# Performance work log

Measured on AMD Instinct MI355X. Metric: run time of the kernel, lower is better.

Reference implementation:

```python
import jax, jax.numpy as jnp
import numpy as np

B = 256       # batch
H = 512       # latent_size == hidden_size == t_channels == o_channels
O_LEN = 512   # decode steps (output_shape[0])


def setup_inputs() -> dict:
    key = jax.random.key(0)
    ks = jax.random.split(key, 7)
    s = 1.0 / np.sqrt(H)
    u = lambda k, shp: jax.random.uniform(k, shp, jnp.float32, -s, s)
    return {
        "z": jax.random.normal(ks[0], (B, H), jnp.float32),
        "W_ih": u(ks[1], (4 * H, H)),   # PyTorch LSTM weight_ih_l0, gate order i,f,g,o
        "W_hh": u(ks[2], (4 * H, H)),
        "b_ih": u(ks[3], (4 * H,)),
        "b_hh": u(ks[4], (4 * H,)),
        "W_last": u(ks[5], (H, H)),     # nn.Linear(hidden_size, o_channels)
        "b_last": u(ks[6], (H,)),
    }


def reference(z, W_ih, W_hh, b_ih, b_hh, W_last, b_last):
    b = b_ih + b_hh

    def step(carry, _):
        x, h, c = carry  # each (B, H)
        gates = x @ W_ih.T + h @ W_hh.T + b  # (B, 4H)
        i, f, g, o = jnp.split(gates, 4, axis=-1)
        c = jax.nn.sigmoid(f) * c + jax.nn.sigmoid(i) * jnp.tanh(g)
        h = jax.nn.sigmoid(o) * jnp.tanh(c)
        y = h @ W_last.T + b_last  # (B, H) -> fed back as next input
        return (y, h, c), y

    # state = (z, z) as (h0, c0); first input x0 = z
    _, ys = jax.lax.scan(step, (z, z, z), None, length=O_LEN)  # ys: (O_LEN, B, H)
    return jnp.transpose(ys, (1, 0, 2))  # (B, O_LEN, H)
```

## Files before the change

kernel.cpp:

```cpp
#include <hip/hip_runtime.h>


#define HH 512
#define TT 512

typedef _Float16 half8 __attribute__((ext_vector_type(8)));
typedef float f32x4 __attribute__((ext_vector_type(4)));

__device__ __forceinline__ float sigm(float x) { return 1.0f / (1.0f + __expf(-x)); }
__device__ __forceinline__ float tanh_(float x) { return 1.0f - 2.0f / (__expf(2.0f * x) + 1.0f); }
__device__ __forceinline__ unsigned short f16b(float x) {
    _Float16 h = (_Float16)x;
    return __builtin_bit_cast(unsigned short, h);
}

__global__ __launch_bounds__(256) void k_weff(const float* __restrict__ Wih,
                                              const float* __restrict__ Whh,
                                              const float* __restrict__ Wlast,
                                              unsigned short* __restrict__ Wbig) {
    __shared__ float wih[16 * 512];
    const int tid = threadIdx.x;
    const int r0 = blockIdx.x * 16;
    for (int i = tid; i < (16 * 512) / 4; i += 256) {
        ((float4*)wih)[i] = ((const float4*)(Wih + (size_t)r0 * 512))[i];
    }
    __syncthreads();
    float acc0[16], acc1[16];
#pragma unroll
    for (int rr = 0; rr < 16; ++rr) { acc0[rr] = 0.f; acc1[rr] = 0.f; }
    const int k0 = tid * 2;
    for (int j = 0; j < 512; ++j) {
        const float2 wl = *(const float2*)(Wlast + (size_t)j * 512 + k0);
#pragma unroll
        for (int rr = 0; rr < 16; ++rr) {
            const float a = wih[rr * 512 + j];
            acc0[rr] += a * wl.x;
            acc1[rr] += a * wl.y;
        }
    }
#pragma unroll
    for (int rr = 0; rr < 16; ++rr) {
        const int gr = r0 + rr;
        const int q = gr >> 9, j = gr & 511;
        const int dst = 80 * (j >> 4) + q * 16 + (j & 15);
        const float v0 = acc0[rr] + Whh[(size_t)gr * 512 + k0];
        const float v1 = acc1[rr] + Whh[(size_t)gr * 512 + k0 + 1];
        Wbig[(size_t)dst * 512 + k0] = f16b(v0);
        Wbig[(size_t)dst * 512 + k0 + 1] = f16b(v1);
    }
}

__global__ __launch_bounds__(256) void k_pack(const float* __restrict__ z,
                                              const float* __restrict__ Wih,
                                              const float* __restrict__ Whh,
                                              const float* __restrict__ bih,
                                              const float* __restrict__ bhh,
                                              const float* __restrict__ Wlast,
                                              const float* __restrict__ blast,
                                              unsigned short* __restrict__ Wbig,
                                              unsigned short* __restrict__ W0big,
                                              float* __restrict__ biasEff,
                                              float* __restrict__ bias0,
                                              unsigned short* __restrict__ hbuf,
                                              unsigned int* __restrict__ counters) {
    const int nthr = gridDim.x * blockDim.x;
    const int gtid = blockIdx.x * blockDim.x + threadIdx.x;
    for (int e = gtid; e < 2560 * 512; e += nthr) {
        const int r = e >> 9, k = e & 511;
        const int s = r / 80, rem = r - s * 80;
        const int tau = rem >> 4, jj = rem & 15;
        const int j = s * 16 + jj;
        if (tau == 4) {
            const unsigned short v = f16b(Wlast[(size_t)j * 512 + k]);
            Wbig[e] = v;
            W0big[e] = v;
        } else {
            const int gr = tau * 512 + j;
            W0big[e] = f16b(Wih[(size_t)gr * 512 + k] + Whh[(size_t)gr * 512 + k]);
        }
    }
    for (int r = gtid; r < 2560; r += nthr) {
        const int s = r / 80, rem = r - s * 80;
        const int tau = rem >> 4, jj = rem & 15;
        const int j = s * 16 + jj;
        if (tau == 4) {
            bias0[r] = blast[j];
            biasEff[r] = blast[j];
        } else {
            const int gr = tau * 512 + j;
            const float base = bih[gr] + bhh[gr];
            float dot = 0.f;
            for (int k = 0; k < 512; ++k) dot += Wih[(size_t)gr * 512 + k] * blast[k];
            bias0[r] = base;
            biasEff[r] = base + dot;
        }
    }
    for (int e = gtid; e < 256 * 512; e += nthr) {
        const int b = e >> 9, k = e & 511;
        const int g = b >> 5, bl = b & 31;
        hbuf[((size_t)(g * 2) * 32 + bl) * 512 + k] = f16b(z[e]);
    }
    for (int e = gtid; e < 512; e += nthr) counters[e] = 0u;
}

__global__ __launch_bounds__(256, 1) void k_lstm(const unsigned short* __restrict__ Wbig,
                                                 const unsigned short* __restrict__ W0big,
                                                 const float* __restrict__ biasEff,
                                                 const float* __restrict__ bias0,
                                                 unsigned short* __restrict__ hbuf,
                                                 unsigned int* __restrict__ counters,
                                                 const float* __restrict__ z,
                                                 float* __restrict__ out) {
    const int g = blockIdx.x & 7;
    const int s = blockIdx.x >> 3;
    const int tid = threadIdx.x;
    const int wave = tid >> 6;
    const int lane = tid & 63;
    const int l15 = lane & 15;
    const int q4 = lane >> 4;

    __shared__ unsigned short hstage[32 * 520];
    __shared__ float gatesL[32 * 68];
    __shared__ float cL[32 * 18];

    const int mbase = (wave >> 1) * 16;
    const int ntile0 = (wave & 1) ? 3 : 0;
    const int ntcount = (wave & 1) ? 2 : 3;

    unsigned short* hb0 = hbuf + (size_t)(g * 2) * 32 * 512;
    unsigned short* hb1 = hb0 + 32 * 512;
    unsigned int* cnt = counters + g * 64;

    for (int idx = tid; idx < 512; idx += 256) {
        const int b = idx >> 4, jj = idx & 15;
        cL[b * 18 + jj] = z[(size_t)(g * 32 + b) * 512 + 16 * s + jj];
    }

    half8 bfrag[3][16];
#pragma unroll
    for (int tt = 0; tt < 3; ++tt) {
        if (tt < ntcount) {
            const int row = 80 * s + (ntile0 + tt) * 16 + l15;
#pragma unroll
            for (int kk = 0; kk < 16; ++kk) {
                bfrag[tt][kk] = *(const half8*)(W0big + (size_t)row * 512 + kk * 32 + q4 * 8);
            }
        }
    }
    float bias0v[3], biasEv[3];
#pragma unroll
    for (int tt = 0; tt < 3; ++tt) {
        if (tt < ntcount) {
            const int r = 80 * s + (ntile0 + tt) * 16 + l15;
            bias0v[tt] = bias0[r];
            biasEv[tt] = biasEff[r];
        } else {
            bias0v[tt] = 0.f;
            biasEv[tt] = 0.f;
        }
    }

    for (int t = 0; t <= 512; ++t) {
        {
            const unsigned short* src = (t & 1) ? hb1 : hb0;
            const char* p = (const char*)src + tid * 16;
            half8 st[8];
            asm volatile(
                "global_load_dwordx4 %0, %8, off sc0 sc1\n\t"
                "global_load_dwordx4 %1, %9, off sc0 sc1\n\t"
                "global_load_dwordx4 %2, %10, off sc0 sc1\n\t"
                "global_load_dwordx4 %3, %11, off sc0 sc1\n\t"
                "global_load_dwordx4 %4, %12, off sc0 sc1\n\t"
                "global_load_dwordx4 %5, %13, off sc0 sc1\n\t"
                "global_load_dwordx4 %6, %14, off sc0 sc1\n\t"
                "global_load_dwordx4 %7, %15, off sc0 sc1\n\t"
                "s_waitcnt vmcnt(0)"
                : "=&v"(st[0]), "=&v"(st[1]), "=&v"(st[2]), "=&v"(st[3]),
                  "=&v"(st[4]), "=&v"(st[5]), "=&v"(st[6]), "=&v"(st[7])
                : "v"(p), "v"(p + 4096), "v"(p + 8192), "v"(p + 12288),
                  "v"(p + 16384), "v"(p + 20480), "v"(p + 24576), "v"(p + 28672)
                : "memory");
#pragma unroll
            for (int i = 0; i < 8; ++i) {
                const int ci = i * 256 + tid;
                const int row = ci >> 6, col = ci & 63;
                *(half8*)(hstage + row * 520 + col * 8) = st[i];
            }
        }
        __syncthreads();

        f32x4 acc[3];
#pragma unroll
        for (int tt = 0; tt < 3; ++tt) {
            const float bv = (t == 0) ? bias0v[tt] : biasEv[tt];
            acc[tt] = (f32x4){bv, bv, bv, bv};
        }
#pragma unroll
        for (int kk = 0; kk < 16; ++kk) {
            const half8 a = *(const half8*)(hstage + (mbase + l15) * 520 + kk * 32 + q4 * 8);
#pragma unroll
            for (int tt = 0; tt < 3; ++tt) {
                if (tt < ntcount)
                    acc[tt] = __builtin_amdgcn_mfma_f32_16x16x32_f16(a, bfrag[tt][kk], acc[tt], 0, 0, 0);
            }
        }

        if ((wave & 1) && t >= 1) {
            const int n = 16 * s + l15;
#pragma unroll
            for (int r = 0; r < 4; ++r) {
                const int m = mbase + q4 * 4 + r;
                const size_t off = (size_t)(g * 32 + m) * (TT * HH) + (size_t)(t - 1) * HH + n;
                out[off] = acc[1][r];
            }
        }
        if (t == 512) break;

        {
            const int nst = (wave & 1) ? 1 : 3;
#pragma unroll
            for (int tt = 0; tt < 3; ++tt) {
                if (tt < nst) {
                    const int col = (ntile0 + tt) * 16 + l15;
#pragma unroll
                    for (int r = 0; r < 4; ++r) {
                        const int m = mbase + q4 * 4 + r;
                        gatesL[m * 68 + col] = acc[tt][r];
                    }
                }
            }
        }
        __syncthreads();

        {
            const int b = tid >> 3, jp = tid & 7;
            const int j0 = jp * 2;
            const float2 iv = *(const float2*)(gatesL + b * 68 + j0);
            const float2 fv = *(const float2*)(gatesL + b * 68 + 16 + j0);
            const float2 gv = *(const float2*)(gatesL + b * 68 + 32 + j0);
            const float2 ov = *(const float2*)(gatesL + b * 68 + 48 + j0);
            float2 cv = *(const float2*)(cL + b * 18 + j0);
            const float c0 = sigm(fv.x) * cv.x + sigm(iv.x) * tanh_(gv.x);
            const float c1 = sigm(fv.y) * cv.y + sigm(iv.y) * tanh_(gv.y);
            const float h0 = sigm(ov.x) * tanh_(c0);
            const float h1 = sigm(ov.y) * tanh_(c1);
            cv.x = c0;
            cv.y = c1;
            *(float2*)(cL + b * 18 + j0) = cv;
            unsigned short* dst = (t & 1) ? hb0 : hb1;
            const unsigned int packed = (unsigned int)f16b(h0) | ((unsigned int)f16b(h1) << 16);
            __hip_atomic_store((unsigned int*)(dst + b * 512 + 16 * s + j0), packed,
                               __ATOMIC_RELAXED, __HIP_MEMORY_SCOPE_AGENT);
        }

        if (t == 0) {
#pragma unroll
            for (int tt = 0; tt < 3; ++tt) {
                if (tt < ntcount) {
                    const int row = 80 * s + (ntile0 + tt) * 16 + l15;
#pragma unroll
                    for (int kk = 0; kk < 16; ++kk) {
                        bfrag[tt][kk] = *(const half8*)(Wbig + (size_t)row * 512 + kk * 32 + q4 * 8);
                    }
                }
            }
        }

        __syncthreads();
        if (tid == 0) {
            __hip_atomic_fetch_add(cnt, 1u, __ATOMIC_RELAXED, __HIP_MEMORY_SCOPE_AGENT);
            const unsigned int target = 32u * (unsigned)(t + 1);
            while (__hip_atomic_load(cnt, __ATOMIC_RELAXED, __HIP_MEMORY_SCOPE_AGENT) < target) {
            }
        }
        __syncthreads();
    }
}

extern "C" void kernel_launch(void* const* d_in, const int* in_sizes, int n_in,
                              void* d_out, int out_size, void* d_ws, size_t ws_size,
                              hipStream_t stream) {
    const float* z = (const float*)d_in[0];
    const float* Wih = (const float*)d_in[1];
    const float* Whh = (const float*)d_in[2];
    const float* bih = (const float*)d_in[3];
    const float* bhh = (const float*)d_in[4];
    const float* Wlast = (const float*)d_in[5];
    const float* blast = (const float*)d_in[6];
    float* out = (float*)d_out;

    char* ws = (char*)d_ws;
    unsigned short* Wbig = (unsigned short*)(ws);
    unsigned short* W0big = (unsigned short*)(ws + 2621440);
    float* biasEff = (float*)(ws + 5242880);
    float* bias0 = (float*)(ws + 5253120);
    unsigned short* hbuf = (unsigned short*)(ws + 5263360);
    unsigned int* counters = (unsigned int*)(ws + 5787648);

    k_weff<<<128, 256, 0, stream>>>(Wih, Whh, Wlast, Wbig);
    k_pack<<<512, 256, 0, stream>>>(z, Wih, Whh, bih, bhh, Wlast, blast, Wbig, W0big, biasEff,
                                    bias0, hbuf, counters);
    k_lstm<<<256, 256, 0, stream>>>(Wbig, W0big, biasEff, bias0, hbuf, counters, z, out);
}
```

Measured before the change: 2.251 ms.

## Keep LSTM gate tiles in registers per wave and halve the persistent block count

Each wave now computes all five 16-column tiles (i, f, g, o and the output projection) for its own hidden slice. The cell update therefore runs directly on MFMA accumulators, with the cell state held in registers instead of going through a shared-memory gates buffer. This removes one __syncthreads and the shared-memory round trip from every recurrent step. The grid shrinks from 256 to 128 blocks, so each group barrier waits for 16 arrivals instead of 32. Output stores move after the inter-block barrier so they can overlap the wait, and the spin loop gets an iteration cap, which risks a stale hidden-state read if the wait ever runs past the cap.

```diff
diff --git a/kernel.cpp b/kernel.cpp
--- a/kernel.cpp
+++ b/kernel.cpp
@@ -112,7 +112,7 @@
                                                  const float* __restrict__ z,
                                                  float* __restrict__ out) {
     const int g = blockIdx.x & 7;
-    const int s = blockIdx.x >> 3;
+    const int pair = blockIdx.x >> 3;
     const int tid = threadIdx.x;
     const int wave = tid >> 6;
     const int lane = tid & 63;
@@ -120,44 +120,36 @@
     const int q4 = lane >> 4;
 
     __shared__ unsigned short hstage[32 * 520];
-    __shared__ float gatesL[32 * 68];
-    __shared__ float cL[32 * 18];
-
-    const int mbase = (wave >> 1) * 16;
-    const int ntile0 = (wave & 1) ? 3 : 0;
-    const int ntcount = (wave & 1) ? 2 : 3;
+
+    const int slice = 2 * pair + (wave >> 1);
+    const int Mbase = (wave & 1) * 16;
+    const int jcol = 16 * slice + l15;
 
     unsigned short* hb0 = hbuf + (size_t)(g * 2) * 32 * 512;
     unsigned short* hb1 = hb0 + 32 * 512;
     unsigned int* cnt = counters + g * 64;
 
-    for (int idx = tid; idx < 512; idx += 256) {
-        const int b = idx >> 4, jj = idx & 15;
-        cL[b * 18 + jj] = z[(size_t)(g * 32 + b) * 512 + 16 * s + jj];
-    }
-
-    half8 bfrag[3][16];
-#pragma unroll
-    for (int tt = 0; tt < 3; ++tt) {
-        if (tt < ntcount) {
-            const int row = 80 * s + (ntile0 + tt) * 16 + l15;
-#pragma unroll
-            for (int kk = 0; kk < 16; ++kk) {
-                bfrag[tt][kk] = *(const half8*)(W0big + (size_t)row * 512 + kk * 32 + q4 * 8);
-            }
-        }
-    }
-    float bias0v[3], biasEv[3];
-#pragma unroll
-    for (int tt = 0; tt < 3; ++tt) {
-        if (tt < ntcount) {
-            const int r = 80 * s + (ntile0 + tt) * 16 + l15;
-            bias0v[tt] = bias0[r];
-            biasEv[tt] = biasEff[r];
-        } else {
-            bias0v[tt] = 0.f;
-            biasEv[tt] = 0.f;
-        }
+    float c_reg[4];
+#pragma unroll
+    for (int r = 0; r < 4; ++r) {
+        c_reg[r] = z[(size_t)(g * 32 + Mbase + q4 * 4 + r) * 512 + jcol];
+    }
+
+    half8 bfrag[5][16];
+#pragma unroll
+    for (int tt = 0; tt < 5; ++tt) {
+        const int row = 80 * slice + tt * 16 + l15;
+#pragma unroll
+        for (int kk = 0; kk < 16; ++kk) {
+            bfrag[tt][kk] = *(const half8*)(W0big + (size_t)row * 512 + kk * 32 + q4 * 8);
+        }
+    }
+    float bias0v[5], biasEv[5];
+#pragma unroll
+    for (int tt = 0; tt < 5; ++tt) {
+        const int r = 80 * slice + tt * 16 + l15;
+        bias0v[tt] = bias0[r];
+        biasEv[tt] = biasEff[r];
     }
 
     for (int t = 0; t <= 512; ++t) {
@@ -189,79 +181,53 @@
         }
         __syncthreads();
 
-        f32x4 acc[3];
-#pragma unroll
-        for (int tt = 0; tt < 3; ++tt) {
+        f32x4 acc[5];
+#pragma unroll
+        for (int tt = 0; tt < 5; ++tt) {
             const float bv = (t == 0) ? bias0v[tt] : biasEv[tt];
             acc[tt] = (f32x4){bv, bv, bv, bv};
         }
 #pragma unroll
         for (int kk = 0; kk < 16; ++kk) {
-            const half8 a = *(const half8*)(hstage + (mbase + l15) * 520 + kk * 32 + q4 * 8);
-#pragma unroll
-            for (int tt = 0; tt < 3; ++tt) {
-                if (tt < ntcount)
-                    acc[tt] = __builtin_amdgcn_mfma_f32_16x16x32_f16(a, bfrag[tt][kk], acc[tt], 0, 0, 0);
-            }
-        }
-
-        if ((wave & 1) && t >= 1) {
-            const int n = 16 * s + l15;
+            const half8 a = *(const half8*)(hstage + (Mbase + l15) * 520 + kk * 32 + q4 * 8);
+#pragma unroll
+            for (int tt = 0; tt < 5; ++tt) {
+                acc[tt] = __builtin_amdgcn_mfma_f32_16x16x32_f16(a, bfrag[tt][kk], acc[tt], 0, 0, 0);
+            }
+        }
+
+        if (t == 512) {
 #pragma unroll
             for (int r = 0; r < 4; ++r) {
-                const int m = mbase + q4 * 4 + r;
-                const size_t off = (size_t)(g * 32 + m) * (TT * HH) + (size_t)(t - 1) * HH + n;
-                out[off] = acc[1][r];
-            }
-        }
-        if (t == 512) break;
+                const size_t off = (size_t)(g * 32 + Mbase + q4 * 4 + r) * (TT * HH) +
+                                   (size_t)(t - 1) * HH + jcol;
+                out[off] = acc[4][r];
+            }
+            break;
+        }
 
         {
-            const int nst = (wave & 1) ? 1 : 3;
-#pragma unroll
-            for (int tt = 0; tt < 3; ++tt) {
-                if (tt < nst) {
-                    const int col = (ntile0 + tt) * 16 + l15;
-#pragma unroll
-                    for (int r = 0; r < 4; ++r) {
-                        const int m = mbase + q4 * 4 + r;
-                        gatesL[m * 68 + col] = acc[tt][r];
-                    }
-                }
-            }
-        }
-        __syncthreads();
-
-        {
-            const int b = tid >> 3, jp = tid & 7;
-            const int j0 = jp * 2;
-            const float2 iv = *(const float2*)(gatesL + b * 68 + j0);
-            const float2 fv = *(const float2*)(gatesL + b * 68 + 16 + j0);
-            const float2 gv = *(const float2*)(gatesL + b * 68 + 32 + j0);
-            const float2 ov = *(const float2*)(gatesL + b * 68 + 48 + j0);
-            float2 cv = *(const float2*)(cL + b * 18 + j0);
-            const float c0 = sigm(fv.x) * cv.x + sigm(iv.x) * tanh_(gv.x);
-            const float c1 = sigm(fv.y) * cv.y + sigm(iv.y) * tanh_(gv.y);
-            const float h0 = sigm(ov.x) * tanh_(c0);
-            const float h1 = sigm(ov.y) * tanh_(c1);
-            cv.x = c0;
-            cv.y = c1;
-            *(float2*)(cL + b * 18 + j0) = cv;
             unsigned short* dst = (t & 1) ? hb0 : hb1;
-            const unsigned int packed = (unsigned int)f16b(h0) | ((unsigned int)f16b(h1) << 16);
-            __hip_atomic_store((unsigned int*)(dst + b * 512 + 16 * s + j0), packed,
-                               __ATOMIC_RELAXED, __HIP_MEMORY_SCOPE_AGENT);
+#pragma unroll
+            for (int r = 0; r < 4; ++r) {
+                const float iv = acc[0][r], fv = acc[1][r], gv = acc[2][r], ov = acc[3][r];
+                const float c0 = sigm(fv) * c_reg[r] + sigm(iv) * tanh_(gv);
+                c_reg[r] = c0;
+                const float h0 = sigm(ov) * tanh_(c0);
+                unsigned short* pp = dst + (size_t)(Mbase + q4 * 4 + r) * 512 + jcol;
+                const unsigned short hv = f16b(h0);
+                asm volatile("global_store_short %0, %1, off sc0 sc1" ::"v"(pp), "v"(hv)
+                             : "memory");
+            }
         }
 
         if (t == 0) {
 #pragma unroll
-            for (int tt = 0; tt < 3; ++tt) {
-                if (tt < ntcount) {
-                    const int row = 80 * s + (ntile0 + tt) * 16 + l15;
-#pragma unroll
-                    for (int kk = 0; kk < 16; ++kk) {
-                        bfrag[tt][kk] = *(const half8*)(Wbig + (size_t)row * 512 + kk * 32 + q4 * 8);
-                    }
+            for (int tt = 0; tt < 4; ++tt) {
+                const int row = 80 * slice + tt * 16 + l15;
+#pragma unroll
+                for (int kk = 0; kk < 16; ++kk) {
+                    bfrag[tt][kk] = *(const half8*)(Wbig + (size_t)row * 512 + kk * 32 + q4 * 8);
                 }
             }
         }
@@ -269,11 +235,22 @@
         __syncthreads();
         if (tid == 0) {
             __hip_atomic_fetch_add(cnt, 1u, __ATOMIC_RELAXED, __HIP_MEMORY_SCOPE_AGENT);
-            const unsigned int target = 32u * (unsigned)(t + 1);
-            while (__hip_atomic_load(cnt, __ATOMIC_RELAXED, __HIP_MEMORY_SCOPE_AGENT) < target) {
+            const unsigned int target = 16u * (unsigned)(t + 1);
+            int guard = 0;
+            while (__hip_atomic_load(cnt, __ATOMIC_RELAXED, __HIP_MEMORY_SCOPE_AGENT) < target &&
+                   ++guard < 65536) {
             }
         }
         __syncthreads();
+
+        if (t >= 1) {
+#pragma unroll
+            for (int r = 0; r < 4; ++r) {
+                const size_t off = (size_t)(g * 32 + Mbase + q4 * 4 + r) * (TT * HH) +
+                                   (size_t)(t - 1) * HH + jcol;
+                out[off] = acc[4][r];
+            }
+        }
     }
 }
 
@@ -300,5 +277,5 @@
     k_weff<<<128, 256, 0, stream>>>(Wih, Whh, Wlast, Wbig);
     k_pack<<<512, 256, 0, stream>>>(z, Wih, Whh, bih, bhh, Wlast, blast, Wbig, W0big, biasEff,
                                     bias0, hbuf, counters);
-    k_lstm<<<256, 256, 0, stream>>>(Wbig, W0big, biasEff, bias0, hbuf, counters, z, out);
-}
+    k_lstm<<<128, 256, 0, stream>>>(Wbig, W0big, biasEff, bias0, hbuf, counters, z, out);
+}
```

Result: slower. 4.918 ms (+118.5%).

## Repartition LSTM blocks into 16 batch groups with two gate slices each

Applied to the files above, without the earlier changes.

Each persistent block now owns 16 batch rows and two 16-column hidden slices, instead of 32 batch rows and one slice. This halves the hidden-state rows each block must reload from global memory every step. It also halves the number of blocks in each group-wide spin barrier, from 32 to 16, to cut per-step synchronisation latency. The spin wait gains an iteration cap, which risks silently proceeding on stale state if a barrier is slow.

```diff
diff --git a/kernel.cpp b/kernel.cpp
--- a/kernel.cpp
+++ b/kernel.cpp
@@ -97,8 +97,8 @@
     }
     for (int e = gtid; e < 256 * 512; e += nthr) {
         const int b = e >> 9, k = e & 511;
-        const int g = b >> 5, bl = b & 31;
-        hbuf[((size_t)(g * 2) * 32 + bl) * 512 + k] = f16b(z[e]);
+        const int g = b >> 4, bl = b & 15;
+        hbuf[(size_t)g * 16384 + bl * 512 + k] = f16b(z[e]);
     }
     for (int e = gtid; e < 512; e += nthr) counters[e] = 0u;
 }
@@ -111,36 +111,38 @@
                                                  unsigned int* __restrict__ counters,
                                                  const float* __restrict__ z,
                                                  float* __restrict__ out) {
-    const int g = blockIdx.x & 7;
-    const int s = blockIdx.x >> 3;
+    const int g = blockIdx.x & 15;
+    const int pair = blockIdx.x >> 4;
     const int tid = threadIdx.x;
     const int wave = tid >> 6;
     const int lane = tid & 63;
     const int l15 = lane & 15;
     const int q4 = lane >> 4;
 
-    __shared__ unsigned short hstage[32 * 520];
-    __shared__ float gatesL[32 * 68];
-    __shared__ float cL[32 * 18];
-
-    const int mbase = (wave >> 1) * 16;
+    __shared__ unsigned short hstage[16 * 520];
+    __shared__ float gatesL[2 * 16 * 68];
+    __shared__ float cL[2 * 16 * 18];
+
+    const int sl = wave >> 1;
+    const int slice = 2 * pair + sl;
     const int ntile0 = (wave & 1) ? 3 : 0;
     const int ntcount = (wave & 1) ? 2 : 3;
 
-    unsigned short* hb0 = hbuf + (size_t)(g * 2) * 32 * 512;
-    unsigned short* hb1 = hb0 + 32 * 512;
-    unsigned int* cnt = counters + g * 64;
+    unsigned short* hb0 = hbuf + (size_t)g * 16384;
+    unsigned short* hb1 = hb0 + 8192;
+    unsigned int* cnt = counters + g * 32;
 
     for (int idx = tid; idx < 512; idx += 256) {
-        const int b = idx >> 4, jj = idx & 15;
-        cL[b * 18 + jj] = z[(size_t)(g * 32 + b) * 512 + 16 * s + jj];
+        const int b = idx >> 5, j0 = idx & 31;
+        const int s2 = j0 >> 4, jj = j0 & 15;
+        cL[(s2 * 16 + b) * 18 + jj] = z[(size_t)(g * 16 + b) * 512 + 32 * pair + j0];
     }
 
     half8 bfrag[3][16];
 #pragma unroll
     for (int tt = 0; tt < 3; ++tt) {
         if (tt < ntcount) {
-            const int row = 80 * s + (ntile0 + tt) * 16 + l15;
+            const int row = 80 * slice + (ntile0 + tt) * 16 + l15;
 #pragma unroll
             for (int kk = 0; kk < 16; ++kk) {
                 bfrag[tt][kk] = *(const half8*)(W0big + (size_t)row * 512 + kk * 32 + q4 * 8);
@@ -151,7 +153,7 @@
 #pragma unroll
     for (int tt = 0; tt < 3; ++tt) {
         if (tt < ntcount) {
-            const int r = 80 * s + (ntile0 + tt) * 16 + l15;
+            const int r = 80 * slice + (ntile0 + tt) * 16 + l15;
             bias0v[tt] = bias0[r];
             biasEv[tt] = biasEff[r];
         } else {
@@ -164,24 +166,18 @@
         {
             const unsigned short* src = (t & 1) ? hb1 : hb0;
             const char* p = (const char*)src + tid * 16;
-            half8 st[8];
+            half8 st[4];
             asm volatile(
-                "global_load_dwordx4 %0, %8, off sc0 sc1\n\t"
-                "global_load_dwordx4 %1, %9, off sc0 sc1\n\t"
-                "global_load_dwordx4 %2, %10, off sc0 sc1\n\t"
-                "global_load_dwordx4 %3, %11, off sc0 sc1\n\t"
-                "global_load_dwordx4 %4, %12, off sc0 sc1\n\t"
-                "global_load_dwordx4 %5, %13, off sc0 sc1\n\t"
-                "global_load_dwordx4 %6, %14, off sc0 sc1\n\t"
-                "global_load_dwordx4 %7, %15, off sc0 sc1\n\t"
+                "global_load_dwordx4 %0, %4, off sc0 sc1\n\t"
+                "global_load_dwordx4 %1, %5, off sc0 sc1\n\t"
+                "global_load_dwordx4 %2, %6, off sc0 sc1\n\t"
+                "global_load_dwordx4 %3, %7, off sc0 sc1\n\t"
                 "s_waitcnt vmcnt(0)"
-                : "=&v"(st[0]), "=&v"(st[1]), "=&v"(st[2]), "=&v"(st[3]),
-                  "=&v"(st[4]), "=&v"(st[5]), "=&v"(st[6]), "=&v"(st[7])
-                : "v"(p), "v"(p + 4096), "v"(p + 8192), "v"(p + 12288),
-                  "v"(p + 16384), "v"(p + 20480), "v"(p + 24576), "v"(p + 28672)
+                : "=&v"(st[0]), "=&v"(st[1]), "=&v"(st[2]), "=&v"(st[3])
+                : "v"(p), "v"(p + 4096), "v"(p + 8192), "v"(p + 12288)
                 : "memory");
 #pragma unroll
-            for (int i = 0; i < 8; ++i) {
+            for (int i = 0; i < 4; ++i) {
                 const int ci = i * 256 + tid;
                 const int row = ci >> 6, col = ci & 63;
                 *(half8*)(hstage + row * 520 + col * 8) = st[i];
@@ -197,7 +193,7 @@
         }
 #pragma unroll
         for (int kk = 0; kk < 16; ++kk) {
-            const half8 a = *(const half8*)(hstage + (mbase + l15) * 520 + kk * 32 + q4 * 8);
+            const half8 a = *(const half8*)(hstage + l15 * 520 + kk * 32 + q4 * 8);
 #pragma unroll
             for (int tt = 0; tt < 3; ++tt) {
                 if (tt < ntcount)
@@ -206,11 +202,12 @@
         }
 
         if ((wave & 1) && t >= 1) {
-            const int n = 16 * s + l15;
+            const int n = 16 * slice + l15;
 #pragma unroll
             for (int r = 0; r < 4; ++r) {
-                const int m = mbase + q4 * 4 + r;
-                const size_t off = (size_t)(g * 32 + m) * (TT * HH) + (size_t)(t - 1) * HH + n;
+                const int m = q4 * 4 + r;
+                const size_t off =
+                    (size_t)(g * 16 + m) * (TT * HH) + (size_t)(t - 1) * HH + n;
                 out[off] = acc[1][r];
             }
         }
@@ -224,8 +221,8 @@
                     const int col = (ntile0 + tt) * 16 + l15;
 #pragma unroll
                     for (int r = 0; r < 4; ++r) {
-                        const int m = mbase + q4 * 4 + r;
-                        gatesL[m * 68 + col] = acc[tt][r];
+                        const int m = q4 * 4 + r;
+                        gatesL[(sl * 16 + m) * 68 + col] = acc[tt][r];
                     }
                 }
             }
@@ -233,23 +230,26 @@
         __syncthreads();
 
         {
-            const int b = tid >> 3, jp = tid & 7;
+            const int b = tid >> 4, jp = tid & 15;
             const int j0 = jp * 2;
-            const float2 iv = *(const float2*)(gatesL + b * 68 + j0);
-            const float2 fv = *(const float2*)(gatesL + b * 68 + 16 + j0);
-            const float2 gv = *(const float2*)(gatesL + b * 68 + 32 + j0);
-            const float2 ov = *(const float2*)(gatesL + b * 68 + 48 + j0);
-            float2 cv = *(const float2*)(cL + b * 18 + j0);
-            const float c0 = sigm(fv.x) * cv.x + sigm(iv.x) * tanh_(gv.x);
-            const float c1 = sigm(fv.y) * cv.y + sigm(iv.y) * tanh_(gv.y);
+            const int s2 = j0 >> 4, jj = j0 & 15;
+            const float* gb = gatesL + (s2 * 16 + b) * 68;
+            const float2 iv = *(const float2*)(gb + jj);
+            const float2 fvv = *(const float2*)(gb + 16 + jj);
+            const float2 gv = *(const float2*)(gb + 32 + jj);
+            const float2 ov = *(const float2*)(gb + 48 + jj);
+            float* cp = cL + (s2 * 16 + b) * 18 + jj;
+            float2 cv = *(const float2*)cp;
+            const float c0 = sigm(fvv.x) * cv.x + sigm(iv.x) * tanh_(gv.x);
+            const float c1 = sigm(fvv.y) * cv.y + sigm(iv.y) * tanh_(gv.y);
             const float h0 = sigm(ov.x) * tanh_(c0);
             const float h1 = sigm(ov.y) * tanh_(c1);
             cv.x = c0;
             cv.y = c1;
-            *(float2*)(cL + b * 18 + j0) = cv;
+            *(float2*)cp = cv;
             unsigned short* dst = (t & 1) ? hb0 : hb1;
             const unsigned int packed = (unsigned int)f16b(h0) | ((unsigned int)f16b(h1) << 16);
-            __hip_atomic_store((unsigned int*)(dst + b * 512 + 16 * s + j0), packed,
+            __hip_atomic_store((unsigned int*)(dst + b * 512 + 32 * pair + j0), packed,
                                __ATOMIC_RELAXED, __HIP_MEMORY_SCOPE_AGENT);
         }
 
@@ -257,7 +257,7 @@
 #pragma unroll
             for (int tt = 0; tt < 3; ++tt) {
                 if (tt < ntcount) {
-                    const int row = 80 * s + (ntile0 + tt) * 16 + l15;
+                    const int row = 80 * slice + (ntile0 + tt) * 16 + l15;
 #pragma unroll
                     for (int kk = 0; kk < 16; ++kk) {
                         bfrag[tt][kk] = *(const half8*)(Wbig + (size_t)row * 512 + kk * 32 + q4 * 8);
@@ -269,8 +269,10 @@
         __syncthreads();
         if (tid == 0) {
             __hip_atomic_fetch_add(cnt, 1u, __ATOMIC_RELAXED, __HIP_MEMORY_SCOPE_AGENT);
-            const unsigned int target = 32u * (unsigned)(t + 1);
-            while (__hip_atomic_load(cnt, __ATOMIC_RELAXED, __HIP_MEMORY_SCOPE_AGENT) < target) {
+            const unsigned int target = 16u * (unsigned)(t + 1);
+            int guard = 0;
+            while (__hip_atomic_load(cnt, __ATOMIC_RELAXED, __HIP_MEMORY_SCOPE_AGENT) < target &&
+                   ++guard < 65536) {
             }
         }
         __syncthreads();
```

Result: faster. 2.026 ms (-10.0%).
